# Optimization experiments

Hardware: AMD Instinct MI355X
Metric: run time of the kernel (lower is better)

Reference implementation:

```python
import jax, jax.numpy as jnp
import numpy as np

B, N, C = 2, 65536, 256
H, D, S = 8, 64, 64  # heads, dim_head, slice_num
INNER = H * D


def setup_inputs() -> dict:
    key = jax.random.key(0)
    ks = jax.random.split(key, 8)
    scale_in = 1.0 / np.sqrt(C)
    scale_d = 1.0 / np.sqrt(D)
    return {
        "x": jax.random.normal(ks[0], (B, N, C), dtype=jnp.float32),
        "W_x": jax.random.uniform(ks[1], (C, INNER), jnp.float32, -scale_in, scale_in),
        "b_x": jax.random.uniform(ks[2], (INNER,), jnp.float32, -scale_in, scale_in),
        "W_fx": jax.random.uniform(ks[3], (C, INNER), jnp.float32, -scale_in, scale_in),
        "b_fx": jax.random.uniform(ks[4], (INNER,), jnp.float32, -scale_in, scale_in),
        "W_slice": jax.random.uniform(ks[5], (D, S), jnp.float32, -scale_d, scale_d),
        "b_slice": jax.random.uniform(ks[6], (S,), jnp.float32, -scale_d, scale_d),
        "temperature": jnp.full((1, H, 1, 1), 0.5, dtype=jnp.float32),
    }


def _split_heads(t):
    # (B, N, H*D) -> (B, H, N, D)
    return t.reshape(B, N, H, D).transpose(0, 2, 1, 3)


def reference(x, W_x, b_x, W_fx, b_fx, W_slice, b_slice, temperature):
    projected_x = _split_heads(x @ W_x + b_x)          # (B,H,N,D)
    fx = _split_heads(x @ W_fx + b_fx)                 # (B,H,N,D)
    slice_proj = projected_x @ W_slice + b_slice       # (B,H,N,S)
    temp = jnp.clip(temperature, 0.5, 5.0)
    slice_weights = jax.nn.softmax(slice_proj / temp, axis=-1)  # (B,H,N,S)
    slice_norm = slice_weights.sum(axis=2)             # (B,H,S)
    normed = slice_weights / (slice_norm[:, :, None, :] + 0.01)
    # weighted token aggregation: (B,H,S,D)
    slice_tokens = jnp.einsum("bhns,bhnd->bhsd", normed, fx)
    return slice_tokens
```

## Files before the change

kernel.cpp:

```cpp
#include <hip/hip_runtime.h>

typedef _Float16 f16;
typedef __attribute__((ext_vector_type(8))) _Float16 f16x8;
typedef __attribute__((ext_vector_type(4))) _Float16 f16x4;
typedef __attribute__((ext_vector_type(4))) float    f32x4;

#define MFMA(a,b,c) __builtin_amdgcn_mfma_f32_16x16x32_f16(a,b,c,0,0,0)

constexpr int Bc = 2, Nc = 65536, Cc = 256, Hc = 8;
constexpr int CHUNK = 512;
constexpr int LDX = 72;
constexpr int LDT = 136;


__device__ __forceinline__ f32x4 splat4(float v) { f32x4 r; r.x=v; r.y=v; r.z=v; r.w=v; return r; }
__device__ __forceinline__ f16x8 pack8(float4 a, float4 b) {
  f16x8 r = { (f16)a.x,(f16)a.y,(f16)a.z,(f16)a.w,(f16)b.x,(f16)b.y,(f16)b.z,(f16)b.w };
  return r;
}

__global__ void prep_a(const float* __restrict__ Wx, const float* __restrict__ Wfx,
                       const float* __restrict__ Wsl, const float* __restrict__ bx,
                       const float* __restrict__ bsl, f16* __restrict__ WC,
                       float* __restrict__ bsp) {
  __shared__ float tile[64][72];
  const int b = blockIdx.x, t = threadIdx.x;
  if (b < 32) {
    const int k0 = (b & 3) * 64, c0 = (b >> 2) * 64;
    const int r = t >> 4, c4 = (t & 15) * 4;
    #pragma unroll
    for (int i = 0; i < 4; ++i) {
      float4 v = *(const float4*)&Wfx[(size_t)(k0 + r + i*16)*512 + c0 + c4];
      tile[r + i*16][c4] = v.x; tile[r + i*16][c4+1] = v.y;
      tile[r + i*16][c4+2] = v.z; tile[r + i*16][c4+3] = v.w;
    }
    __syncthreads();
    const int cl = t >> 2, kq = t & 3;
    const int col = c0 + cl, h = col >> 6, n = col & 63;
    f16 tmp[16];
    #pragma unroll
    for (int j = 0; j < 16; ++j) tmp[j] = (f16)tile[kq*16 + j][cl];
    f16* dst = WC + (size_t)(h*128 + n)*256 + k0 + kq*16;
    *(f16x8*)dst       = *(f16x8*)&tmp[0];
    *(f16x8*)(dst + 8) = *(f16x8*)&tmp[8];
  } else if (b < 96) {
    const int bb = b - 32;
    const int h = bb >> 3, k0 = (bb & 7) * 32;
    const int k = t & 31, sq = t >> 5;
    float accs[8];
    #pragma unroll
    for (int j = 0; j < 8; ++j) accs[j] = 0.f;
    for (int d = 0; d < 64; ++d) {
      float a = Wx[(size_t)(k0 + k)*512 + h*64 + d];
      #pragma unroll
      for (int j = 0; j < 8; ++j) accs[j] += a * Wsl[d*64 + sq*8 + j];
    }
    #pragma unroll
    for (int j = 0; j < 8; ++j)
      WC[(size_t)(h*128 + 64 + sq*8 + j)*256 + k0 + k] = (f16)accs[j];
  } else {
    for (int u = t; u < 512; u += 256) {
      int h = u >> 6, s = u & 63;
      float a = bsl[s];
      for (int d = 0; d < 64; ++d) a += bx[h*64 + d] * Wsl[d*64 + s];
      bsp[h*64 + s] = a;
    }
  }
}

__global__ __launch_bounds__(256, 2)
void fused_main(const float* __restrict__ x,   const float* __restrict__ bfx,
                const float* __restrict__ bsp, const float* __restrict__ temp,
                const f16* __restrict__ WC,    float* __restrict__ Tg,
                float* __restrict__ normg) {
  __shared__ alignas(16) char smem[2 * 128 * LDX * 2];
  f16* sm_x   = (f16*)smem;
  f16* sm_w   = (f16*)(smem + 128*LDX*2);
  f16* sm_fxT = sm_x;
  f16* sm_wT  = sm_w;

  const int j    = blockIdx.x;
  const int xcd  = j & 7, slot = j >> 3;
  const int chunk = xcd * 32 + (slot >> 3);
  const int h     = slot & 7;

  const int tid = threadIdx.x;
  const int wv = tid >> 6, lane = tid & 63, quad = lane >> 4, ln = lane & 15;
  const int wm = wv >> 1, wn = wv & 1;
  const long tokBase = (long)chunk * CHUNK;
  const int b  = (int)(tokBase >> 16);
  const int bh = b * Hc + h;

  const float tc = fminf(fmaxf(temp[h], 0.5f), 5.0f);
  const float k2 = 1.44269504f / tc;

  float bv[4];
  {
    const float* bb = (wn == 0) ? (bfx + h*64) : (bsp + h*64);
    #pragma unroll
    for (int nt = 0; nt < 4; ++nt) bv[nt] = bb[nt*16 + ln];
  }

  f32x4 Tacc[2][2];
  #pragma unroll
  for (int i = 0; i < 2; ++i) { Tacc[i][0] = splat4(0.f); Tacc[i][1] = splat4(0.f); }
  float nacc[4] = {0.f, 0.f, 0.f, 0.f};
  const int ci = wv >> 1, cj = wv & 1;

  const f16* WCh = WC + (size_t)h * 128 * 256;

  const int r0 = tid >> 2, seg = tid & 3;
  const int wrow = tid >> 1, whalf = tid & 1;

  float4 xr[8]; f16x8 wr[4];
  auto loadx = [&](int m0, int kb) {
    const float* p = x + (tokBase + (long)m0*128 + r0)*Cc + kb*64 + seg*16;
    xr[0] = *(const float4*)p;        xr[1] = *(const float4*)(p + 4);
    xr[2] = *(const float4*)(p + 8);  xr[3] = *(const float4*)(p + 12);
    p += 64 * Cc;
    xr[4] = *(const float4*)p;        xr[5] = *(const float4*)(p + 4);
    xr[6] = *(const float4*)(p + 8);  xr[7] = *(const float4*)(p + 12);
  };
  auto loadw = [&](int kb) {
    const f16* p = WCh + wrow*256 + kb*64 + whalf*32;
    wr[0] = *(const f16x8*)p;         wr[1] = *(const f16x8*)(p + 8);
    wr[2] = *(const f16x8*)(p + 16);  wr[3] = *(const f16x8*)(p + 24);
  };

  loadx(0, 0); loadw(0);

  for (int m0 = 0; m0 < 4; ++m0) {
    f32x4 acc[4][4];
    #pragma unroll
    for (int mt = 0; mt < 4; ++mt)
      #pragma unroll
      for (int nt = 0; nt < 4; ++nt) acc[mt][nt] = splat4(bv[nt]);

    for (int kb = 0; kb < 4; ++kb) {
      __syncthreads();
      *(f16x8*)&sm_x[r0*LDX + seg*16]          = pack8(xr[0], xr[1]);
      *(f16x8*)&sm_x[r0*LDX + seg*16 + 8]      = pack8(xr[2], xr[3]);
      *(f16x8*)&sm_x[(r0+64)*LDX + seg*16]     = pack8(xr[4], xr[5]);
      *(f16x8*)&sm_x[(r0+64)*LDX + seg*16 + 8] = pack8(xr[6], xr[7]);
      *(f16x8*)&sm_w[wrow*LDX + whalf*32]      = wr[0];
      *(f16x8*)&sm_w[wrow*LDX + whalf*32 +  8] = wr[1];
      *(f16x8*)&sm_w[wrow*LDX + whalf*32 + 16] = wr[2];
      *(f16x8*)&sm_w[wrow*LDX + whalf*32 + 24] = wr[3];
      { int nkb = kb + 1, nm0 = m0;
        if (nkb == 4) { nkb = 0; ++nm0; }
        if (nm0 < 4) { loadx(nm0, nkb); loadw(nkb); } }
      __syncthreads();
      #pragma unroll
      for (int ks = 0; ks < 2; ++ks) {
        f16x8 af[4], bf[4];
        #pragma unroll
        for (int mt = 0; mt < 4; ++mt)
          af[mt] = *(const f16x8*)&sm_x[(wm*64 + mt*16 + ln)*LDX + ks*32 + quad*8];
        #pragma unroll
        for (int nt = 0; nt < 4; ++nt)
          bf[nt] = *(const f16x8*)&sm_w[(wn*64 + nt*16 + ln)*LDX + ks*32 + quad*8];
        #pragma unroll
        for (int mt = 0; mt < 4; ++mt)
          #pragma unroll
          for (int nt = 0; nt < 4; ++nt)
            acc[mt][nt] = MFMA(af[mt], bf[nt], acc[mt][nt]);
      }
    }
    __syncthreads();

    if (wn == 0) {
      #pragma unroll
      for (int mt = 0; mt < 4; ++mt)
        #pragma unroll
        for (int nt = 0; nt < 4; ++nt) {
          f16x4 v = { (f16)acc[mt][nt][0], (f16)acc[mt][nt][1],
                      (f16)acc[mt][nt][2], (f16)acc[mt][nt][3] };
          *(f16x4*)&sm_fxT[(nt*16 + ln)*LDT + wm*64 + mt*16 + quad*4] = v;
        }
    } else {
      #pragma unroll
      for (int mt = 0; mt < 4; ++mt) {
        float e[4][4], wout[4][4];
        #pragma unroll
        for (int nt = 0; nt < 4; ++nt)
          #pragma unroll
          for (int rg = 0; rg < 4; ++rg)
            e[nt][rg] = exp2f(acc[mt][nt][rg] * k2);
        #pragma unroll
        for (int rg = 0; rg < 4; ++rg) {
          float rs = e[0][rg] + e[1][rg] + e[2][rg] + e[3][rg];
          #pragma unroll
          for (int dd = 1; dd < 16; dd <<= 1) rs += __shfl_xor(rs, dd, 64);
          float inv = 1.0f / rs;
          #pragma unroll
          for (int nt = 0; nt < 4; ++nt) {
            wout[nt][rg] = e[nt][rg] * inv;
            nacc[nt] += wout[nt][rg];
          }
        }
        #pragma unroll
        for (int nt = 0; nt < 4; ++nt) {
          f16x4 v = { (f16)wout[nt][0], (f16)wout[nt][1],
                      (f16)wout[nt][2], (f16)wout[nt][3] };
          *(f16x4*)&sm_wT[(nt*16 + ln)*LDT + wm*64 + mt*16 + quad*4] = v;
        }
      }
    }
    __syncthreads();

    #pragma unroll
    for (int ks = 0; ks < 4; ++ks) {
      f16x8 a0 = *(const f16x8*)&sm_wT [(ci*32 +      ln)*LDT + ks*32 + quad*8];
      f16x8 a1 = *(const f16x8*)&sm_wT [(ci*32 + 16 + ln)*LDT + ks*32 + quad*8];
      f16x8 b0 = *(const f16x8*)&sm_fxT[(cj*32 +      ln)*LDT + ks*32 + quad*8];
      f16x8 b1 = *(const f16x8*)&sm_fxT[(cj*32 + 16 + ln)*LDT + ks*32 + quad*8];
      Tacc[0][0] = MFMA(a0, b0, Tacc[0][0]);
      Tacc[0][1] = MFMA(a0, b1, Tacc[0][1]);
      Tacc[1][0] = MFMA(a1, b0, Tacc[1][0]);
      Tacc[1][1] = MFMA(a1, b1, Tacc[1][1]);
    }
  }

  float* Tb = Tg + bh * 4096;
  #pragma unroll
  for (int mt2 = 0; mt2 < 2; ++mt2)
    #pragma unroll
    for (int nt2 = 0; nt2 < 2; ++nt2)
      #pragma unroll
      for (int rg = 0; rg < 4; ++rg) {
        int s = ci*32 + mt2*16 + quad*4 + rg;
        int d = cj*32 + nt2*16 + ln;
        atomicAdd(&Tb[s*64 + d], Tacc[mt2][nt2][rg]);
      }
  if (wn == 1) {
    #pragma unroll
    for (int nt = 0; nt < 4; ++nt) {
      float v = nacc[nt];
      v += __shfl_xor(v, 16, 64);
      v += __shfl_xor(v, 32, 64);
      if (lane < 16) atomicAdd(&normg[bh*64 + nt*16 + ln], v);
    }
  }
}

__global__ void finalize(const float* __restrict__ Tg, const float* __restrict__ normg,
                         float* __restrict__ out) {
  int i = blockIdx.x * 256 + threadIdx.x;
  out[i] = Tg[i] / (normg[i >> 6] + 0.01f);
}

extern "C" void kernel_launch(void* const* d_in, const int* in_sizes, int n_in,
                              void* d_out, int out_size, void* d_ws, size_t ws_size,
                              hipStream_t stream) {
  const float* x    = (const float*)d_in[0];
  const float* Wx   = (const float*)d_in[1];
  const float* bx   = (const float*)d_in[2];
  const float* Wfx  = (const float*)d_in[3];
  const float* bfx  = (const float*)d_in[4];
  const float* Wsl  = (const float*)d_in[5];
  const float* bsl  = (const float*)d_in[6];
  const float* temp = (const float*)d_in[7];
  float* out = (float*)d_out;

  float* Tg    = (float*)d_ws;
  float* normg = Tg + 16 * 4096;
  f16*   WC    = (f16*)((char*)d_ws + 266240);
  float* bsp   = (float*)((char*)d_ws + 790528);

  hipMemsetAsync(d_ws, 0, 266240, stream);
  prep_a    <<<97, 256, 0, stream>>>(Wx, Wfx, Wsl, bx, bsl, WC, bsp);
  fused_main<<<2048, 256, 0, stream>>>(x, bfx, bsp, temp, WC, Tg, normg);
  finalize  <<<256, 256, 0, stream>>>(Tg, normg, out);
}
```

Before: 345.7 us.

## Load GEMM operands directly from global memory into registers, dropping LDS staging

```diff
diff --git a/kernel.cpp b/kernel.cpp
--- a/kernel.cpp
+++ b/kernel.cpp
@@ -9,7 +9,6 @@
 
 constexpr int Bc = 2, Nc = 65536, Cc = 256, Hc = 8;
 constexpr int CHUNK = 512;
-constexpr int LDX = 72;
 constexpr int LDT = 136;
 
 
@@ -68,16 +67,13 @@
   }
 }
 
-__global__ __launch_bounds__(256, 2)
+__global__ __launch_bounds__(256, 1)
 void fused_main(const float* __restrict__ x,   const float* __restrict__ bfx,
                 const float* __restrict__ bsp, const float* __restrict__ temp,
                 const f16* __restrict__ WC,    float* __restrict__ Tg,
                 float* __restrict__ normg) {
-  __shared__ alignas(16) char smem[2 * 128 * LDX * 2];
-  f16* sm_x   = (f16*)smem;
-  f16* sm_w   = (f16*)(smem + 128*LDX*2);
-  f16* sm_fxT = sm_x;
-  f16* sm_wT  = sm_w;
+  __shared__ alignas(16) f16 sm_fxT[64 * LDT];
+  __shared__ alignas(16) f16 sm_wT [64 * LDT];
 
   const int j    = blockIdx.x;
   const int xcd  = j & 7, slot = j >> 3;
@@ -86,7 +82,6 @@
 
   const int tid = threadIdx.x;
   const int wv = tid >> 6, lane = tid & 63, quad = lane >> 4, ln = lane & 15;
-  const int wm = wv >> 1, wn = wv & 1;
   const long tokBase = (long)chunk * CHUNK;
   const int b  = (int)(tokBase >> 16);
   const int bh = b * Hc + h;
@@ -94,12 +89,11 @@
   const float tc = fminf(fmaxf(temp[h], 0.5f), 5.0f);
   const float k2 = 1.44269504f / tc;
 
-  float bv[4];
-  {
-    const float* bb = (wn == 0) ? (bfx + h*64) : (bsp + h*64);
-    #pragma unroll
-    for (int nt = 0; nt < 4; ++nt) bv[nt] = bb[nt*16 + ln];
-  }
+  float bv[8];
+  #pragma unroll
+  for (int nt = 0; nt < 4; ++nt) bv[nt]     = bfx[h*64 + nt*16 + ln];
+  #pragma unroll
+  for (int nt = 0; nt < 4; ++nt) bv[4 + nt] = bsp[h*64 + nt*16 + ln];
 
   f32x4 Tacc[2][2];
   #pragma unroll
@@ -108,102 +102,72 @@
   const int ci = wv >> 1, cj = wv & 1;
 
   const f16* WCh = WC + (size_t)h * 128 * 256;
-
-  const int r0 = tid >> 2, seg = tid & 3;
-  const int wrow = tid >> 1, whalf = tid & 1;
-
-  float4 xr[8]; f16x8 wr[4];
-  auto loadx = [&](int m0, int kb) {
-    const float* p = x + (tokBase + (long)m0*128 + r0)*Cc + kb*64 + seg*16;
-    xr[0] = *(const float4*)p;        xr[1] = *(const float4*)(p + 4);
-    xr[2] = *(const float4*)(p + 8);  xr[3] = *(const float4*)(p + 12);
-    p += 64 * Cc;
-    xr[4] = *(const float4*)p;        xr[5] = *(const float4*)(p + 4);
-    xr[6] = *(const float4*)(p + 8);  xr[7] = *(const float4*)(p + 12);
-  };
-  auto loadw = [&](int kb) {
-    const f16* p = WCh + wrow*256 + kb*64 + whalf*32;
-    wr[0] = *(const f16x8*)p;         wr[1] = *(const f16x8*)(p + 8);
-    wr[2] = *(const f16x8*)(p + 16);  wr[3] = *(const f16x8*)(p + 24);
-  };
-
-  loadx(0, 0); loadw(0);
+  const float* xrow  = x + (tokBase + wv*32 + ln) * (long)Cc + quad*8;
+  const f16*   wrowq = WCh + ln*256 + quad*8;
 
   for (int m0 = 0; m0 < 4; ++m0) {
-    f32x4 acc[4][4];
-    #pragma unroll
-    for (int mt = 0; mt < 4; ++mt)
-      #pragma unroll
-      for (int nt = 0; nt < 4; ++nt) acc[mt][nt] = splat4(bv[nt]);
-
+    f32x4 acc[2][8];
+    #pragma unroll
+    for (int mt = 0; mt < 2; ++mt)
+      #pragma unroll
+      for (int nt = 0; nt < 8; ++nt) acc[mt][nt] = splat4(bv[nt]);
+
+    #pragma unroll
     for (int kb = 0; kb < 4; ++kb) {
-      __syncthreads();
-      *(f16x8*)&sm_x[r0*LDX + seg*16]          = pack8(xr[0], xr[1]);
-      *(f16x8*)&sm_x[r0*LDX + seg*16 + 8]      = pack8(xr[2], xr[3]);
-      *(f16x8*)&sm_x[(r0+64)*LDX + seg*16]     = pack8(xr[4], xr[5]);
-      *(f16x8*)&sm_x[(r0+64)*LDX + seg*16 + 8] = pack8(xr[6], xr[7]);
-      *(f16x8*)&sm_w[wrow*LDX + whalf*32]      = wr[0];
-      *(f16x8*)&sm_w[wrow*LDX + whalf*32 +  8] = wr[1];
-      *(f16x8*)&sm_w[wrow*LDX + whalf*32 + 16] = wr[2];
-      *(f16x8*)&sm_w[wrow*LDX + whalf*32 + 24] = wr[3];
-      { int nkb = kb + 1, nm0 = m0;
-        if (nkb == 4) { nkb = 0; ++nm0; }
-        if (nm0 < 4) { loadx(nm0, nkb); loadw(nkb); } }
-      __syncthreads();
       #pragma unroll
       for (int ks = 0; ks < 2; ++ks) {
-        f16x8 af[4], bf[4];
-        #pragma unroll
-        for (int mt = 0; mt < 4; ++mt)
-          af[mt] = *(const f16x8*)&sm_x[(wm*64 + mt*16 + ln)*LDX + ks*32 + quad*8];
-        #pragma unroll
-        for (int nt = 0; nt < 4; ++nt)
-          bf[nt] = *(const f16x8*)&sm_w[(wn*64 + nt*16 + ln)*LDX + ks*32 + quad*8];
-        #pragma unroll
-        for (int mt = 0; mt < 4; ++mt)
-          #pragma unroll
-          for (int nt = 0; nt < 4; ++nt)
-            acc[mt][nt] = MFMA(af[mt], bf[nt], acc[mt][nt]);
-      }
-    }
+        const int ko = kb*64 + ks*32;
+        f16x8 af0, af1;
+        {
+          const float* p = xrow + ko;
+          af0 = pack8(*(const float4*)p, *(const float4*)(p + 4));
+          p += 16 * Cc;
+          af1 = pack8(*(const float4*)p, *(const float4*)(p + 4));
+        }
+        f16x8 bf[8];
+        #pragma unroll
+        for (int nt = 0; nt < 8; ++nt)
+          bf[nt] = *(const f16x8*)(wrowq + nt*(16*256) + ko);
+        #pragma unroll
+        for (int nt = 0; nt < 8; ++nt) {
+          acc[0][nt] = MFMA(af0, bf[nt], acc[0][nt]);
+          acc[1][nt] = MFMA(af1, bf[nt], acc[1][nt]);
+        }
+      }
+    }
+
     __syncthreads();
 
-    if (wn == 0) {
-      #pragma unroll
-      for (int mt = 0; mt < 4; ++mt)
+    #pragma unroll
+    for (int mt = 0; mt < 2; ++mt) {
+      #pragma unroll
+      for (int nt = 0; nt < 4; ++nt) {
+        f32x4 a = acc[mt][nt];
+        f16x4 v = { (f16)a[0], (f16)a[1], (f16)a[2], (f16)a[3] };
+        *(f16x4*)&sm_fxT[(nt*16 + ln)*LDT + wv*32 + mt*16 + quad*4] = v;
+      }
+      float e[4][4];
+      #pragma unroll
+      for (int nt = 0; nt < 4; ++nt)
+        #pragma unroll
+        for (int rg = 0; rg < 4; ++rg)
+          e[nt][rg] = exp2f(acc[mt][4 + nt][rg] * k2);
+      #pragma unroll
+      for (int rg = 0; rg < 4; ++rg) {
+        float rs = e[0][rg] + e[1][rg] + e[2][rg] + e[3][rg];
+        #pragma unroll
+        for (int dd = 1; dd < 16; dd <<= 1) rs += __shfl_xor(rs, dd, 64);
+        float inv = 1.0f / rs;
         #pragma unroll
         for (int nt = 0; nt < 4; ++nt) {
-          f16x4 v = { (f16)acc[mt][nt][0], (f16)acc[mt][nt][1],
-                      (f16)acc[mt][nt][2], (f16)acc[mt][nt][3] };
-          *(f16x4*)&sm_fxT[(nt*16 + ln)*LDT + wm*64 + mt*16 + quad*4] = v;
+          e[nt][rg] *= inv;
+          nacc[nt] += e[nt][rg];
         }
-    } else {
-      #pragma unroll
-      for (int mt = 0; mt < 4; ++mt) {
-        float e[4][4], wout[4][4];
-        #pragma unroll
-        for (int nt = 0; nt < 4; ++nt)
-          #pragma unroll
-          for (int rg = 0; rg < 4; ++rg)
-            e[nt][rg] = exp2f(acc[mt][nt][rg] * k2);
-        #pragma unroll
-        for (int rg = 0; rg < 4; ++rg) {
-          float rs = e[0][rg] + e[1][rg] + e[2][rg] + e[3][rg];
-          #pragma unroll
-          for (int dd = 1; dd < 16; dd <<= 1) rs += __shfl_xor(rs, dd, 64);
-          float inv = 1.0f / rs;
-          #pragma unroll
-          for (int nt = 0; nt < 4; ++nt) {
-            wout[nt][rg] = e[nt][rg] * inv;
-            nacc[nt] += wout[nt][rg];
-          }
-        }
-        #pragma unroll
-        for (int nt = 0; nt < 4; ++nt) {
-          f16x4 v = { (f16)wout[nt][0], (f16)wout[nt][1],
-                      (f16)wout[nt][2], (f16)wout[nt][3] };
-          *(f16x4*)&sm_wT[(nt*16 + ln)*LDT + wm*64 + mt*16 + quad*4] = v;
-        }
+      }
+      #pragma unroll
+      for (int nt = 0; nt < 4; ++nt) {
+        f16x4 v = { (f16)e[nt][0], (f16)e[nt][1], (f16)e[nt][2], (f16)e[nt][3] };
+        *(f16x4*)&sm_wT[(nt*16 + ln)*LDT + wv*32 + mt*16 + quad*4] = v;
       }
     }
     __syncthreads();
@@ -219,6 +183,8 @@
       Tacc[1][0] = MFMA(a1, b0, Tacc[1][0]);
       Tacc[1][1] = MFMA(a1, b1, Tacc[1][1]);
     }
+
+    xrow += 128 * Cc;
   }
 
   float* Tb = Tg + bh * 4096;
@@ -232,14 +198,12 @@
         int d = cj*32 + nt2*16 + ln;
         atomicAdd(&Tb[s*64 + d], Tacc[mt2][nt2][rg]);
       }
-  if (wn == 1) {
-    #pragma unroll
-    for (int nt = 0; nt < 4; ++nt) {
-      float v = nacc[nt];
-      v += __shfl_xor(v, 16, 64);
-      v += __shfl_xor(v, 32, 64);
-      if (lane < 16) atomicAdd(&normg[bh*64 + nt*16 + ln], v);
-    }
+  #pragma unroll
+  for (int nt = 0; nt < 4; ++nt) {
+    float v = nacc[nt];
+    v += __shfl_xor(v, 16, 64);
+    v += __shfl_xor(v, 32, 64);
+    if (lane < 16) atomicAdd(&normg[bh*64 + nt*16 + ln], v);
   }
 }
 
```

Result: slower. 671.2 us (+94.2%).

## Double-buffer LDS tiles with two-deep register prefetch and one barrier per step

Applied to the files above, without the earlier changes.

```diff
diff --git a/kernel.cpp b/kernel.cpp
--- a/kernel.cpp
+++ b/kernel.cpp
@@ -9,8 +9,8 @@
 
 constexpr int Bc = 2, Nc = 65536, Cc = 256, Hc = 8;
 constexpr int CHUNK = 512;
-constexpr int LDX = 72;
-constexpr int LDT = 136;
+constexpr int LDX = 68;
+constexpr int LDT = 132;
 
 
 __device__ __forceinline__ f32x4 splat4(float v) { f32x4 r; r.x=v; r.y=v; r.z=v; r.w=v; return r; }
@@ -73,11 +73,13 @@
                 const float* __restrict__ bsp, const float* __restrict__ temp,
                 const f16* __restrict__ WC,    float* __restrict__ Tg,
                 float* __restrict__ normg) {
-  __shared__ alignas(16) char smem[2 * 128 * LDX * 2];
-  f16* sm_x   = (f16*)smem;
-  f16* sm_w   = (f16*)(smem + 128*LDX*2);
-  f16* sm_fxT = sm_x;
-  f16* sm_wT  = sm_w;
+  __shared__ alignas(16) char smem[4 * 128 * LDX * 2];
+  f16* X0 = (f16*)smem;
+  f16* W0 = X0 + 128 * LDX;
+  f16* X1 = W0 + 128 * LDX;
+  f16* W1 = X1 + 128 * LDX;
+  f16* sm_fxT = X1;
+  f16* sm_wT  = W1;
 
   const int j    = blockIdx.x;
   const int xcd  = j & 7, slot = j >> 3;
@@ -126,8 +128,23 @@
     wr[0] = *(const f16x8*)p;         wr[1] = *(const f16x8*)(p + 8);
     wr[2] = *(const f16x8*)(p + 16);  wr[3] = *(const f16x8*)(p + 24);
   };
+  auto store_tile = [&](int p) {
+    f16* sx = p ? X1 : X0;
+    f16* sw = p ? W1 : W0;
+    *(f16x8*)&sx[r0*LDX + seg*16]          = pack8(xr[0], xr[1]);
+    *(f16x8*)&sx[r0*LDX + seg*16 + 8]      = pack8(xr[2], xr[3]);
+    *(f16x8*)&sx[(r0+64)*LDX + seg*16]     = pack8(xr[4], xr[5]);
+    *(f16x8*)&sx[(r0+64)*LDX + seg*16 + 8] = pack8(xr[6], xr[7]);
+    *(f16x8*)&sw[wrow*LDX + whalf*32]      = wr[0];
+    *(f16x8*)&sw[wrow*LDX + whalf*32 +  8] = wr[1];
+    *(f16x8*)&sw[wrow*LDX + whalf*32 + 16] = wr[2];
+    *(f16x8*)&sw[wrow*LDX + whalf*32 + 24] = wr[3];
+  };
 
   loadx(0, 0); loadw(0);
+  store_tile(0);
+  loadx(0, 1); loadw(1);
+  __syncthreads();
 
   for (int m0 = 0; m0 < 4; ++m0) {
     f32x4 acc[4][4];
@@ -136,35 +153,42 @@
       #pragma unroll
       for (int nt = 0; nt < 4; ++nt) acc[mt][nt] = splat4(bv[nt]);
 
+    #pragma unroll
     for (int kb = 0; kb < 4; ++kb) {
-      __syncthreads();
-      *(f16x8*)&sm_x[r0*LDX + seg*16]          = pack8(xr[0], xr[1]);
-      *(f16x8*)&sm_x[r0*LDX + seg*16 + 8]      = pack8(xr[2], xr[3]);
-      *(f16x8*)&sm_x[(r0+64)*LDX + seg*16]     = pack8(xr[4], xr[5]);
-      *(f16x8*)&sm_x[(r0+64)*LDX + seg*16 + 8] = pack8(xr[6], xr[7]);
-      *(f16x8*)&sm_w[wrow*LDX + whalf*32]      = wr[0];
-      *(f16x8*)&sm_w[wrow*LDX + whalf*32 +  8] = wr[1];
-      *(f16x8*)&sm_w[wrow*LDX + whalf*32 + 16] = wr[2];
-      *(f16x8*)&sm_w[wrow*LDX + whalf*32 + 24] = wr[3];
-      { int nkb = kb + 1, nm0 = m0;
-        if (nkb == 4) { nkb = 0; ++nm0; }
-        if (nm0 < 4) { loadx(nm0, nkb); loadw(nkb); } }
-      __syncthreads();
-      #pragma unroll
-      for (int ks = 0; ks < 2; ++ks) {
-        f16x8 af[4], bf[4];
-        #pragma unroll
-        for (int mt = 0; mt < 4; ++mt)
-          af[mt] = *(const f16x8*)&sm_x[(wm*64 + mt*16 + ln)*LDX + ks*32 + quad*8];
+      const int t = m0*4 + kb;
+      if (t > 0) __syncthreads();
+      const f16* sx = (t & 1) ? X1 : X0;
+      const f16* sw = (t & 1) ? W1 : W0;
+
+      f16x8 af[4], bf[4];
+      #pragma unroll
+      for (int mt = 0; mt < 4; ++mt)
+        af[mt] = *(const f16x8*)&sx[(wm*64 + mt*16 + ln)*LDX + quad*8];
+      #pragma unroll
+      for (int nt = 0; nt < 4; ++nt)
+        bf[nt] = *(const f16x8*)&sw[(wn*64 + nt*16 + ln)*LDX + quad*8];
+
+      if (t + 1 < 16) store_tile((t + 1) & 1);
+      if (t + 2 < 16) { loadx((t + 2) >> 2, (t + 2) & 3);
+                        loadw((t + 2) & 3); }
+
+      #pragma unroll
+      for (int mt = 0; mt < 4; ++mt)
         #pragma unroll
         for (int nt = 0; nt < 4; ++nt)
-          bf[nt] = *(const f16x8*)&sm_w[(wn*64 + nt*16 + ln)*LDX + ks*32 + quad*8];
-        #pragma unroll
-        for (int mt = 0; mt < 4; ++mt)
-          #pragma unroll
-          for (int nt = 0; nt < 4; ++nt)
-            acc[mt][nt] = MFMA(af[mt], bf[nt], acc[mt][nt]);
-      }
+          acc[mt][nt] = MFMA(af[mt], bf[nt], acc[mt][nt]);
+
+      #pragma unroll
+      for (int mt = 0; mt < 4; ++mt)
+        af[mt] = *(const f16x8*)&sx[(wm*64 + mt*16 + ln)*LDX + 32 + quad*8];
+      #pragma unroll
+      for (int nt = 0; nt < 4; ++nt)
+        bf[nt] = *(const f16x8*)&sw[(wn*64 + nt*16 + ln)*LDX + 32 + quad*8];
+      #pragma unroll
+      for (int mt = 0; mt < 4; ++mt)
+        #pragma unroll
+        for (int nt = 0; nt < 4; ++nt)
+          acc[mt][nt] = MFMA(af[mt], bf[nt], acc[mt][nt]);
     }
     __syncthreads();
 
```

Result: slower. 614.2 us (+77.7%).
